# Performance work log

Measured on AMD Instinct MI355X. Metric: run time of the kernel, lower is better.

## Reference

```python
import jax, jax.numpy as jnp
import numpy as np

N = 10000       # nodes
E = 320000      # edges
D = 256         # feature dim (out_channels)
L = 5           # num_layers


def setup_inputs() -> dict:
    key = jax.random.key(0)
    ks = jax.random.split(key, 8)
    x = jax.random.normal(ks[0], (N, D), dtype=jnp.float32)
    edge_index = jax.random.randint(ks[1], (2, E), 0, N, dtype=jnp.int64)
    edge_attr = jax.random.uniform(ks[2], (E,), dtype=jnp.float32)
    s = 1.0 / np.sqrt(D)
    # per-layer message transform weights [L, D, D]
    weight = jax.random.uniform(ks[3], (L, D, D), minval=-s, maxval=s, dtype=jnp.float32)
    # GRUCell parameters (torch layout: [3D, D] rows = r, z, n)
    w_ih = jax.random.uniform(ks[4], (3 * D, D), minval=-s, maxval=s, dtype=jnp.float32)
    w_hh = jax.random.uniform(ks[5], (3 * D, D), minval=-s, maxval=s, dtype=jnp.float32)
    b_ih = jax.random.uniform(ks[6], (3 * D,), minval=-s, maxval=s, dtype=jnp.float32)
    b_hh = jax.random.uniform(ks[7], (3 * D,), minval=-s, maxval=s, dtype=jnp.float32)
    return {"x": x, "edge_index": edge_index, "edge_attr": edge_attr,
            "weight": weight, "w_ih": w_ih, "w_hh": w_hh,
            "b_ih": b_ih, "b_hh": b_hh}


def _gru_cell(inp, h, w_ih, w_hh, b_ih, b_hh):
    # torch.nn.GRUCell math
    gi = inp @ w_ih.T + b_ih    # [N, 3D]
    gh = h @ w_hh.T + b_hh      # [N, 3D]
    i_r, i_z, i_n = jnp.split(gi, 3, axis=-1)
    h_r, h_z, h_n = jnp.split(gh, 3, axis=-1)
    r = jax.nn.sigmoid(i_r + h_r)
    z = jax.nn.sigmoid(i_z + h_z)
    n = jnp.tanh(i_n + r * h_n)
    return (1.0 - z) * n + z * h


def reference(x, edge_index, edge_attr, weight, w_ih, w_hh, b_ih, b_hh):
    src, dst = edge_index[0], edge_index[1]
    h = x
    for l in range(L):
        m = h @ weight[l]                                   # [N, D]
        msg = m[src] * edge_attr[:, None]                   # [E, D]
        agg = jax.ops.segment_sum(msg, dst, num_segments=N)  # [N, D]
        h = _gru_cell(agg, h, w_ih, w_hh, b_ih, b_hh)
    return h
```

## Files before the change

kernel.cpp:

```cpp
#include <hip/hip_runtime.h>
#include <hip/hip_bf16.h>

#define NN 10000
#define NPAD 10048
#define EE 320000
#define DD 256
#define LL 5

typedef __bf16 bf16x8 __attribute__((ext_vector_type(8)));
typedef __bf16 bf16x4 __attribute__((ext_vector_type(4)));
typedef float f32x4 __attribute__((ext_vector_type(4)));

__device__ __forceinline__ void gload_lds16(const void* g, void* l) {
    __builtin_amdgcn_global_load_lds(
        (const __attribute__((address_space(1))) void*)g,
        (__attribute__((address_space(3))) void*)l, 16, 0, 0);
}


__global__ void prep_k(const float* __restrict__ w_hh, const float* __restrict__ x,
                       __bf16* __restrict__ whhb,
                       float* __restrict__ hb, __bf16* __restrict__ hbfA,
                       __bf16* __restrict__ hbfB, __bf16* __restrict__ aggb,
                       int* __restrict__ deg) {
    int i = blockIdx.x * blockDim.x + threadIdx.x;
    if (i < NN * DD) { float v = x[i]; hb[i] = v; hbfA[i] = (__bf16)v; }
    if (i < 768 * 256) whhb[i] = (__bf16)w_hh[i];
    if (i < (NPAD - NN) * DD) {
        hbfA[NN * DD + i] = (__bf16)0.f;
        hbfB[NN * DD + i] = (__bf16)0.f;
        aggb[NN * DD + i] = (__bf16)0.f;
    }
    if (i < NN) deg[i] = 0;
}

__global__ void hist_k(const int* __restrict__ dst, int* __restrict__ deg) {
    int e = blockIdx.x * blockDim.x + threadIdx.x;
    if (e < EE) atomicAdd(&deg[dst[e]], 1);
}

__global__ void scan_k(const int* __restrict__ deg, int* __restrict__ row_start,
                       int* __restrict__ cursor) {
    __shared__ int sums[1024];
    const int CH = 10;
    int t = threadIdx.x;
    int base = t * CH;
    int loc[CH];
    int s = 0;
#pragma unroll
    for (int i = 0; i < CH; i++) {
        int v = (base + i < NN) ? deg[base + i] : 0;
        loc[i] = s;
        s += v;
    }
    sums[t] = s;
    __syncthreads();
    for (int off = 1; off < 1024; off <<= 1) {
        int v = (t >= off) ? sums[t - off] : 0;
        __syncthreads();
        sums[t] += v;
        __syncthreads();
    }
    int pre = (t == 0) ? 0 : sums[t - 1];
#pragma unroll
    for (int i = 0; i < CH; i++) {
        int idx = base + i;
        if (idx < NN) {
            int v = pre + loc[i];
            row_start[idx] = v;
            cursor[idx] = v;
        }
    }
    if (t == 1023) row_start[NN] = sums[1023];
}

__global__ void fill_k(const int* __restrict__ ei, const float* __restrict__ attr,
                       int* __restrict__ cursor, int* __restrict__ ssrc,
                       float* __restrict__ sattr) {
    int e = blockIdx.x * blockDim.x + threadIdx.x;
    if (e < EE) {
        int dv = ei[EE + e];
        int p = atomicAdd(&cursor[dv], 1);
        ssrc[p] = ei[e];
        sattr[p] = attr[e];
    }
}


__global__ __launch_bounds__(256)
void beff32_k(const float* __restrict__ wih, const float* __restrict__ W,
              __bf16* __restrict__ beff) {
    __shared__ float As[16][68];
    __shared__ float Bs[16][68];
    int l = blockIdx.z;
    const float* Wl = W + (size_t)l * DD * DD;
    __bf16* Cl = beff + (size_t)l * 768 * DD;
    int tid = threadIdx.x;
    int tx = tid & 15, ty = tid >> 4;
    int jBase = blockIdx.x * 64;
    int tBase = blockIdx.y * 64;
    int lr = tid >> 2, lq = tid & 3;
    float acc[4][4];
#pragma unroll
    for (int i = 0; i < 4; i++)
#pragma unroll
        for (int j = 0; j < 4; j++) acc[i][j] = 0.f;

    for (int k0 = 0; k0 < DD; k0 += 16) {
        float4 av = *(const float4*)(wih + (size_t)(jBase + lr) * DD + k0 + lq * 4);
        float4 bv = *(const float4*)(Wl + (size_t)(tBase + lr) * DD + k0 + lq * 4);
        __syncthreads();
        As[lq * 4 + 0][lr] = av.x; As[lq * 4 + 1][lr] = av.y;
        As[lq * 4 + 2][lr] = av.z; As[lq * 4 + 3][lr] = av.w;
        Bs[lq * 4 + 0][lr] = bv.x; Bs[lq * 4 + 1][lr] = bv.y;
        Bs[lq * 4 + 2][lr] = bv.z; Bs[lq * 4 + 3][lr] = bv.w;
        __syncthreads();
#pragma unroll
        for (int kk = 0; kk < 16; kk++) {
            float a0 = As[kk][ty * 4 + 0], a1 = As[kk][ty * 4 + 1];
            float a2 = As[kk][ty * 4 + 2], a3 = As[kk][ty * 4 + 3];
            float b0 = Bs[kk][tx * 4 + 0], b1 = Bs[kk][tx * 4 + 1];
            float b2 = Bs[kk][tx * 4 + 2], b3 = Bs[kk][tx * 4 + 3];
            acc[0][0] += a0 * b0; acc[0][1] += a0 * b1; acc[0][2] += a0 * b2; acc[0][3] += a0 * b3;
            acc[1][0] += a1 * b0; acc[1][1] += a1 * b1; acc[1][2] += a1 * b2; acc[1][3] += a1 * b3;
            acc[2][0] += a2 * b0; acc[2][1] += a2 * b1; acc[2][2] += a2 * b2; acc[2][3] += a2 * b3;
            acc[3][0] += a3 * b0; acc[3][1] += a3 * b1; acc[3][2] += a3 * b2; acc[3][3] += a3 * b3;
        }
    }
#pragma unroll
    for (int i = 0; i < 4; i++) {
        int j = jBase + ty * 4 + i;
        bf16x4 o;
        o[0] = (__bf16)acc[i][0]; o[1] = (__bf16)acc[i][1];
        o[2] = (__bf16)acc[i][2]; o[3] = (__bf16)acc[i][3];
        *(bf16x4*)(Cl + (size_t)j * DD + tBase + tx * 4) = o;
    }
}


__global__ __launch_bounds__(256)
void aggregate_bf_k(const __bf16* __restrict__ hsrc, const int* __restrict__ row_start,
                    const int* __restrict__ ssrc, const float* __restrict__ sattr,
                    __bf16* __restrict__ aggb) {
    __shared__ int sIdx[4][64];
    __shared__ float sAtt[4][64];
    int w = threadIdx.x >> 6, lane = threadIdx.x & 63;
    int n = blockIdx.x * 4 + w;
    int s0 = row_start[n], s1 = row_start[n + 1];
    int half = lane >> 5;
    int c8 = (lane & 31) * 8;

    float acc[8] = {0.f, 0.f, 0.f, 0.f, 0.f, 0.f, 0.f, 0.f};

    for (int base = s0; base < s1; base += 64) {
        int cnt = min(64, s1 - base);
        if (lane < cnt) {
            sIdx[w][lane] = ssrc[base + lane];
            sAtt[w][lane] = sattr[base + lane];
        }
        int t = 0;
        for (; t + 8 <= cnt; t += 8) {
#pragma unroll
            for (int u = 0; u < 4; u++) {
                int e = t + u * 2 + half;
                int s = sIdx[w][e];
                float ww = sAtt[w][e];
                bf16x8 v = *(const bf16x8*)(hsrc + (size_t)s * DD + c8);
#pragma unroll
                for (int i = 0; i < 8; i++) acc[i] += (float)v[i] * ww;
            }
        }
        for (; t + 2 <= cnt; t += 2) {
            int e = t + half;
            int s = sIdx[w][e];
            float ww = sAtt[w][e];
            bf16x8 v = *(const bf16x8*)(hsrc + (size_t)s * DD + c8);
#pragma unroll
            for (int i = 0; i < 8; i++) acc[i] += (float)v[i] * ww;
        }
        if (t < cnt && half == 0) {
            int s = sIdx[w][t];
            float ww = sAtt[w][t];
            bf16x8 v = *(const bf16x8*)(hsrc + (size_t)s * DD + c8);
#pragma unroll
            for (int i = 0; i < 8; i++) acc[i] += (float)v[i] * ww;
        }
    }

#pragma unroll
    for (int i = 0; i < 8; i++) acc[i] += __shfl_xor(acc[i], 32, 64);

    if (half == 0) {
        bf16x8 o;
#pragma unroll
        for (int i = 0; i < 8; i++) o[i] = (__bf16)acc[i];
        *(bf16x8*)(aggb + (size_t)n * DD + c8) = o;
    }
}


__global__ __launch_bounds__(512, 2)
void gru_mfma_k(const __bf16* __restrict__ aggb, const __bf16* __restrict__ hbf,
                const float* __restrict__ hin,
                const __bf16* __restrict__ bihw, const __bf16* __restrict__ whh,
                const float* __restrict__ b_ih, const float* __restrict__ b_hh,
                float* __restrict__ hout, __bf16* __restrict__ hbfout) {
    __shared__ __bf16 sA[2][2][64][32];
    __shared__ __bf16 sB[6][2][64][32];
    int tid = threadIdx.x;
    int wave = tid >> 6, lane = tid & 63;
    int ln = lane & 15, quad = lane >> 4;
    int nodeBlock = blockIdx.x * 64;
    int colBlock = blockIdx.y * 64;
    int nf = wave & 3;
    int ch = (wave >> 2) * 32;
    int r4 = lane >> 2;
    int kb = (lane & 3) * 8;

    f32x4 acc[6][2] = {};

    for (int k0 = 0; k0 < DD; k0 += 64) {
        __syncthreads();
#pragma unroll
        for (int ii = 0; ii < 8; ii++) {
            int idx = wave * 8 + ii;
            const __bf16* src;
            __bf16* dst;
            if (idx < 16) {
                int mat = idx >> 3;
                int ksub = (idx >> 2) & 1;
                int rg = idx & 3;
                const __bf16* A = mat ? hbf : aggb;
                src = A + (size_t)(nodeBlock + rg * 16 + r4) * DD + k0 + ksub * 32 + kb;
                dst = &sA[mat][ksub][rg * 16][0];
            } else {
                int j = idx - 16;
                int g6 = j >> 3;
                int ksub = (j >> 2) & 1;
                int rg = j & 3;
                const __bf16* B = (g6 < 3) ? bihw : whh;
                int brow = (g6 % 3) * 256 + colBlock + rg * 16 + r4;
                src = B + (size_t)brow * DD + k0 + ksub * 32 + kb;
                dst = &sB[g6][ksub][rg * 16][0];
            }
            gload_lds16(src, dst);
        }
        __syncthreads();

#pragma unroll
        for (int ksub = 0; ksub < 2; ksub++) {
            bf16x8 aA = *(const bf16x8*)&sA[0][ksub][nf * 16 + ln][quad * 8];
            bf16x8 aH = *(const bf16x8*)&sA[1][ksub][nf * 16 + ln][quad * 8];
#pragma unroll
            for (int g = 0; g < 3; g++) {
#pragma unroll
                for (int cc = 0; cc < 2; cc++) {
                    bf16x8 bI = *(const bf16x8*)&sB[g][ksub][ch + cc * 16 + ln][quad * 8];
                    bf16x8 bH = *(const bf16x8*)&sB[3 + g][ksub][ch + cc * 16 + ln][quad * 8];
                    acc[g][cc] = __builtin_amdgcn_mfma_f32_16x16x32_bf16(aA, bI, acc[g][cc], 0, 0, 0);
                    acc[3 + g][cc] = __builtin_amdgcn_mfma_f32_16x16x32_bf16(aH, bH, acc[3 + g][cc], 0, 0, 0);
                }
            }
        }
    }

#pragma unroll
    for (int r = 0; r < 4; r++) {
        int n = nodeBlock + nf * 16 + quad * 4 + r;
        if (n >= NN) continue;
#pragma unroll
        for (int cc = 0; cc < 2; cc++) {
            int d = colBlock + ch + cc * 16 + ln;
            float ir = acc[0][cc][r] + b_ih[d];
            float iz = acc[1][cc][r] + b_ih[d + 256];
            float in_ = acc[2][cc][r] + b_ih[d + 512];
            float hr = acc[3][cc][r] + b_hh[d];
            float hz = acc[4][cc][r] + b_hh[d + 256];
            float hn = acc[5][cc][r] + b_hh[d + 512];
            float rr = 1.f / (1.f + __expf(-(ir + hr)));
            float zz = 1.f / (1.f + __expf(-(iz + hz)));
            float ax = in_ + rr * hn;
            float e2 = __expf(-2.f * ax);
            float nnv = 2.f / (1.f + e2) - 1.f;
            float hp = hin[(size_t)n * DD + d];
            float o = (1.f - zz) * nnv + zz * hp;
            hout[(size_t)n * DD + d] = o;
            hbfout[(size_t)n * DD + d] = (__bf16)o;
        }
    }
}


extern "C" void kernel_launch(void* const* d_in, const int* in_sizes, int n_in,
                              void* d_out, int out_size, void* d_ws, size_t ws_size,
                              hipStream_t stream) {
    const float* x = (const float*)d_in[0];
    const int* edge_index = (const int*)d_in[1];
    const float* edge_attr = (const float*)d_in[2];
    const float* weight = (const float*)d_in[3];
    const float* w_ih = (const float*)d_in[4];
    const float* w_hh = (const float*)d_in[5];
    const float* b_ih = (const float*)d_in[6];
    const float* b_hh = (const float*)d_in[7];

    size_t off = 0;
    char* base = (char*)d_ws;
    auto carve = [&](size_t bytes) -> void* {
        void* p = base + off;
        off += (bytes + 255) & ~(size_t)255;
        return p;
    };
    float* hb = (float*)carve((size_t)NPAD * DD * 4);
    __bf16* hbfA = (__bf16*)carve((size_t)NPAD * DD * 2);
    __bf16* hbfB = (__bf16*)carve((size_t)NPAD * DD * 2);
    __bf16* aggb = (__bf16*)carve((size_t)NPAD * DD * 2);
    __bf16* whhb = (__bf16*)carve((size_t)768 * DD * 2);
    __bf16* beff = (__bf16*)carve((size_t)LL * 768 * DD * 2);
    int* deg = (int*)carve((size_t)NN * 4);
    int* row_start = (int*)carve((size_t)(NN + 1) * 4);
    int* cursor = (int*)carve((size_t)NN * 4);
    int* ssrc = (int*)carve((size_t)EE * 4);
    float* sattr = (float*)carve((size_t)EE * 4);
    (void)ws_size;

    prep_k<<<(NN * DD + 255) / 256, 256, 0, stream>>>(w_hh, x, whhb, hb, hbfA, hbfB,
                                                      aggb, deg);
    hist_k<<<(EE + 255) / 256, 256, 0, stream>>>(edge_index + EE, deg);
    scan_k<<<1, 1024, 0, stream>>>(deg, row_start, cursor);
    fill_k<<<(EE + 255) / 256, 256, 0, stream>>>(edge_index, edge_attr, cursor, ssrc, sattr);
    beff32_k<<<dim3(12, 4, LL), 256, 0, stream>>>(w_ih, weight, beff);

    float* hA = hb;
    float* hB = (float*)d_out;
    __bf16* hbfIn = hbfA;
    __bf16* hbfOut = hbfB;
    for (int l = 0; l < LL; l++) {
        aggregate_bf_k<<<2500, 256, 0, stream>>>(hbfIn, row_start, ssrc, sattr, aggb);
        gru_mfma_k<<<dim3(157, 4), 512, 0, stream>>>(aggb, hbfIn, hA,
                                                     beff + (size_t)l * 768 * DD, whhb,
                                                     b_ih, b_hh, hB, hbfOut);
        float* t = hA; hA = hB; hB = t;
        __bf16* tb = hbfIn; hbfIn = hbfOut; hbfOut = tb;
    }
}
```

Baseline: 356.7 us.

## Fuse edge aggregation into GRU MFMA kernel, keeping aggregates in LDS

Merges the per-layer aggregation and GRU GEMM kernels into one. Each block gathers neighbour features for 64 nodes into shared memory and preloads the bf16 hidden tile with direct global-to-LDS loads. It then runs the six gate GEMMs with MFMA, reading weight fragments straight from global memory. This removes the bf16 aggregate buffer round trip and one launch per layer. In exchange, the gather is repeated by both column blocks, each wave walks 8 nodes serially, and far fewer waves are available for the latency-bound gather.

```diff
diff --git a/kernel.cpp b/kernel.cpp
--- a/kernel.cpp
+++ b/kernel.cpp
@@ -21,15 +21,13 @@
 __global__ void prep_k(const float* __restrict__ w_hh, const float* __restrict__ x,
                        __bf16* __restrict__ whhb,
                        float* __restrict__ hb, __bf16* __restrict__ hbfA,
-                       __bf16* __restrict__ hbfB, __bf16* __restrict__ aggb,
-                       int* __restrict__ deg) {
+                       __bf16* __restrict__ hbfB, int* __restrict__ deg) {
     int i = blockIdx.x * blockDim.x + threadIdx.x;
     if (i < NN * DD) { float v = x[i]; hb[i] = v; hbfA[i] = (__bf16)v; }
     if (i < 768 * 256) whhb[i] = (__bf16)w_hh[i];
     if (i < (NPAD - NN) * DD) {
         hbfA[NN * DD + i] = (__bf16)0.f;
         hbfB[NN * DD + i] = (__bf16)0.f;
-        aggb[NN * DD + i] = (__bf16)0.f;
     }
     if (i < NN) deg[i] = 0;
 }
@@ -138,128 +136,111 @@
 }
 
 
-__global__ __launch_bounds__(256)
-void aggregate_bf_k(const __bf16* __restrict__ hsrc, const int* __restrict__ row_start,
-                    const int* __restrict__ ssrc, const float* __restrict__ sattr,
-                    __bf16* __restrict__ aggb) {
-    __shared__ int sIdx[4][64];
-    __shared__ float sAtt[4][64];
-    int w = threadIdx.x >> 6, lane = threadIdx.x & 63;
-    int n = blockIdx.x * 4 + w;
-    int s0 = row_start[n], s1 = row_start[n + 1];
-    int half = lane >> 5;
-    int c8 = (lane & 31) * 8;
-
-    float acc[8] = {0.f, 0.f, 0.f, 0.f, 0.f, 0.f, 0.f, 0.f};
-
-    for (int base = s0; base < s1; base += 64) {
-        int cnt = min(64, s1 - base);
-        if (lane < cnt) {
-            sIdx[w][lane] = ssrc[base + lane];
-            sAtt[w][lane] = sattr[base + lane];
-        }
-        int t = 0;
-        for (; t + 8 <= cnt; t += 8) {
-#pragma unroll
-            for (int u = 0; u < 4; u++) {
-                int e = t + u * 2 + half;
-                int s = sIdx[w][e];
-                float ww = sAtt[w][e];
-                bf16x8 v = *(const bf16x8*)(hsrc + (size_t)s * DD + c8);
-#pragma unroll
-                for (int i = 0; i < 8; i++) acc[i] += (float)v[i] * ww;
-            }
-        }
-        for (; t + 2 <= cnt; t += 2) {
-            int e = t + half;
-            int s = sIdx[w][e];
-            float ww = sAtt[w][e];
-            bf16x8 v = *(const bf16x8*)(hsrc + (size_t)s * DD + c8);
-#pragma unroll
-            for (int i = 0; i < 8; i++) acc[i] += (float)v[i] * ww;
-        }
-        if (t < cnt && half == 0) {
-            int s = sIdx[w][t];
-            float ww = sAtt[w][t];
-            bf16x8 v = *(const bf16x8*)(hsrc + (size_t)s * DD + c8);
-#pragma unroll
-            for (int i = 0; i < 8; i++) acc[i] += (float)v[i] * ww;
-        }
-    }
-
-#pragma unroll
-    for (int i = 0; i < 8; i++) acc[i] += __shfl_xor(acc[i], 32, 64);
-
-    if (half == 0) {
-        bf16x8 o;
-#pragma unroll
-        for (int i = 0; i < 8; i++) o[i] = (__bf16)acc[i];
-        *(bf16x8*)(aggb + (size_t)n * DD + c8) = o;
-    }
-}
-
-
-__global__ __launch_bounds__(512, 2)
-void gru_mfma_k(const __bf16* __restrict__ aggb, const __bf16* __restrict__ hbf,
-                const float* __restrict__ hin,
-                const __bf16* __restrict__ bihw, const __bf16* __restrict__ whh,
-                const float* __restrict__ b_ih, const float* __restrict__ b_hh,
-                float* __restrict__ hout, __bf16* __restrict__ hbfout) {
-    __shared__ __bf16 sA[2][2][64][32];
-    __shared__ __bf16 sB[6][2][64][32];
+__global__ __launch_bounds__(512, 4)
+void fused_layer_k(const __bf16* __restrict__ hbf, const float* __restrict__ hin,
+                   const int* __restrict__ row_start, const int* __restrict__ ssrc,
+                   const float* __restrict__ sattr,
+                   const __bf16* __restrict__ bihw, const __bf16* __restrict__ whh,
+                   const float* __restrict__ b_ih, const float* __restrict__ b_hh,
+                   float* __restrict__ hout, __bf16* __restrict__ hbfout) {
+    __shared__ __bf16 aggT[8][64][32];
+    __shared__ __bf16 hT[8][64][32];
+    __shared__ int sIdx[8][64];
+    __shared__ float sAtt[8][64];
+
     int tid = threadIdx.x;
     int wave = tid >> 6, lane = tid & 63;
     int ln = lane & 15, quad = lane >> 4;
     int nodeBlock = blockIdx.x * 64;
-    int colBlock = blockIdx.y * 64;
-    int nf = wave & 3;
-    int ch = (wave >> 2) * 32;
     int r4 = lane >> 2;
     int kb = (lane & 3) * 8;
 
-    f32x4 acc[6][2] = {};
-
-    for (int k0 = 0; k0 < DD; k0 += 64) {
-        __syncthreads();
-#pragma unroll
-        for (int ii = 0; ii < 8; ii++) {
-            int idx = wave * 8 + ii;
-            const __bf16* src;
-            __bf16* dst;
-            if (idx < 16) {
-                int mat = idx >> 3;
-                int ksub = (idx >> 2) & 1;
-                int rg = idx & 3;
-                const __bf16* A = mat ? hbf : aggb;
-                src = A + (size_t)(nodeBlock + rg * 16 + r4) * DD + k0 + ksub * 32 + kb;
-                dst = &sA[mat][ksub][rg * 16][0];
-            } else {
-                int j = idx - 16;
-                int g6 = j >> 3;
-                int ksub = (j >> 2) & 1;
-                int rg = j & 3;
-                const __bf16* B = (g6 < 3) ? bihw : whh;
-                int brow = (g6 % 3) * 256 + colBlock + rg * 16 + r4;
-                src = B + (size_t)brow * DD + k0 + ksub * 32 + kb;
-                dst = &sB[g6][ksub][rg * 16][0];
+#pragma unroll
+    for (int ii = 0; ii < 4; ii++) {
+        int idx = wave * 4 + ii;
+        int rg = idx >> 3;
+        int ksub = idx & 7;
+        const __bf16* src = hbf + (size_t)(nodeBlock + rg * 16 + r4) * DD + ksub * 32 + kb;
+        gload_lds16(src, &hT[ksub][rg * 16][0]);
+    }
+
+    int half = lane >> 5;
+    int c8 = (lane & 31) * 8;
+    int L = lane & 31;
+    for (int nn = 0; nn < 8; nn++) {
+        int nl = wave * 8 + nn;
+        int n = nodeBlock + nl;
+        float acc8[8] = {0.f, 0.f, 0.f, 0.f, 0.f, 0.f, 0.f, 0.f};
+        if (n < NN) {
+            int s0 = row_start[n], s1 = row_start[n + 1];
+            for (int base = s0; base < s1; base += 64) {
+                int cnt = min(64, s1 - base);
+                if (lane < cnt) {
+                    sIdx[wave][lane] = ssrc[base + lane];
+                    sAtt[wave][lane] = sattr[base + lane];
+                }
+                int t = 0;
+                for (; t + 8 <= cnt; t += 8) {
+#pragma unroll
+                    for (int u = 0; u < 4; u++) {
+                        int e = t + u * 2 + half;
+                        int s = sIdx[wave][e];
+                        float ww = sAtt[wave][e];
+                        bf16x8 v = *(const bf16x8*)(hbf + (size_t)s * DD + c8);
+#pragma unroll
+                        for (int i = 0; i < 8; i++) acc8[i] += (float)v[i] * ww;
+                    }
+                }
+                for (; t + 2 <= cnt; t += 2) {
+                    int e = t + half;
+                    int s = sIdx[wave][e];
+                    float ww = sAtt[wave][e];
+                    bf16x8 v = *(const bf16x8*)(hbf + (size_t)s * DD + c8);
+#pragma unroll
+                    for (int i = 0; i < 8; i++) acc8[i] += (float)v[i] * ww;
+                }
+                if (t < cnt && half == 0) {
+                    int s = sIdx[wave][t];
+                    float ww = sAtt[wave][t];
+                    bf16x8 v = *(const bf16x8*)(hbf + (size_t)s * DD + c8);
+#pragma unroll
+                    for (int i = 0; i < 8; i++) acc8[i] += (float)v[i] * ww;
+                }
             }
-            gload_lds16(src, dst);
-        }
-        __syncthreads();
-
-#pragma unroll
-        for (int ksub = 0; ksub < 2; ksub++) {
-            bf16x8 aA = *(const bf16x8*)&sA[0][ksub][nf * 16 + ln][quad * 8];
-            bf16x8 aH = *(const bf16x8*)&sA[1][ksub][nf * 16 + ln][quad * 8];
-#pragma unroll
-            for (int g = 0; g < 3; g++) {
-#pragma unroll
-                for (int cc = 0; cc < 2; cc++) {
-                    bf16x8 bI = *(const bf16x8*)&sB[g][ksub][ch + cc * 16 + ln][quad * 8];
-                    bf16x8 bH = *(const bf16x8*)&sB[3 + g][ksub][ch + cc * 16 + ln][quad * 8];
-                    acc[g][cc] = __builtin_amdgcn_mfma_f32_16x16x32_bf16(aA, bI, acc[g][cc], 0, 0, 0);
-                    acc[3 + g][cc] = __builtin_amdgcn_mfma_f32_16x16x32_bf16(aH, bH, acc[3 + g][cc], 0, 0, 0);
-                }
+#pragma unroll
+            for (int i = 0; i < 8; i++) acc8[i] += __shfl_xor(acc8[i], 32, 64);
+        }
+        if (half == 0) {
+            bf16x8 o;
+#pragma unroll
+            for (int i = 0; i < 8; i++) o[i] = (__bf16)acc8[i];
+            *(bf16x8*)&aggT[L >> 2][nl][(L & 3) * 8] = o;
+        }
+    }
+    __syncthreads();
+
+    int nf = wave & 3;
+    int cg = wave >> 2;
+    int colAbs = blockIdx.y * 128 + cg * 64;
+
+    f32x4 acc[6][4] = {};
+
+    const __bf16* pI = bihw + (size_t)(colAbs + ln) * DD + quad * 8;
+    const __bf16* pH = whh + (size_t)(colAbs + ln) * DD + quad * 8;
+
+    for (int ksub = 0; ksub < 8; ksub++) {
+        bf16x8 aA = *(const bf16x8*)&aggT[ksub][nf * 16 + ln][quad * 8];
+        bf16x8 aH = *(const bf16x8*)&hT[ksub][nf * 16 + ln][quad * 8];
+        int ko = ksub * 32;
+#pragma unroll
+        for (int g = 0; g < 3; g++) {
+#pragma unroll
+            for (int cc = 0; cc < 4; cc++) {
+                size_t roff = (size_t)(g * 256 + cc * 16) * DD + ko;
+                bf16x8 bI = *(const bf16x8*)(pI + roff);
+                bf16x8 bH = *(const bf16x8*)(pH + roff);
+                acc[g][cc] = __builtin_amdgcn_mfma_f32_16x16x32_bf16(aA, bI, acc[g][cc], 0, 0, 0);
+                acc[3 + g][cc] = __builtin_amdgcn_mfma_f32_16x16x32_bf16(aH, bH, acc[3 + g][cc], 0, 0, 0);
             }
         }
     }
@@ -269,8 +250,8 @@
         int n = nodeBlock + nf * 16 + quad * 4 + r;
         if (n >= NN) continue;
 #pragma unroll
-        for (int cc = 0; cc < 2; cc++) {
-            int d = colBlock + ch + cc * 16 + ln;
+        for (int cc = 0; cc < 4; cc++) {
+            int d = colAbs + cc * 16 + ln;
             float ir = acc[0][cc][r] + b_ih[d];
             float iz = acc[1][cc][r] + b_ih[d + 256];
             float in_ = acc[2][cc][r] + b_ih[d + 512];
@@ -313,7 +294,6 @@
     float* hb = (float*)carve((size_t)NPAD * DD * 4);
     __bf16* hbfA = (__bf16*)carve((size_t)NPAD * DD * 2);
     __bf16* hbfB = (__bf16*)carve((size_t)NPAD * DD * 2);
-    __bf16* aggb = (__bf16*)carve((size_t)NPAD * DD * 2);
     __bf16* whhb = (__bf16*)carve((size_t)768 * DD * 2);
     __bf16* beff = (__bf16*)carve((size_t)LL * 768 * DD * 2);
     int* deg = (int*)carve((size_t)NN * 4);
@@ -323,8 +303,7 @@
     float* sattr = (float*)carve((size_t)EE * 4);
     (void)ws_size;
 
-    prep_k<<<(NN * DD + 255) / 256, 256, 0, stream>>>(w_hh, x, whhb, hb, hbfA, hbfB,
-                                                      aggb, deg);
+    prep_k<<<(NN * DD + 255) / 256, 256, 0, stream>>>(w_hh, x, whhb, hb, hbfA, hbfB, deg);
     hist_k<<<(EE + 255) / 256, 256, 0, stream>>>(edge_index + EE, deg);
     scan_k<<<1, 1024, 0, stream>>>(deg, row_start, cursor);
     fill_k<<<(EE + 255) / 256, 256, 0, stream>>>(edge_index, edge_attr, cursor, ssrc, sattr);
@@ -335,10 +314,9 @@
     __bf16* hbfIn = hbfA;
     __bf16* hbfOut = hbfB;
     for (int l = 0; l < LL; l++) {
-        aggregate_bf_k<<<2500, 256, 0, stream>>>(hbfIn, row_start, ssrc, sattr, aggb);
-        gru_mfma_k<<<dim3(157, 4), 512, 0, stream>>>(aggb, hbfIn, hA,
-                                                     beff + (size_t)l * 768 * DD, whhb,
-                                                     b_ih, b_hh, hB, hbfOut);
+        fused_layer_k<<<dim3(157, 2), 512, 0, stream>>>(hbfIn, hA, row_start, ssrc, sattr,
+                                                        beff + (size_t)l * 768 * DD, whhb,
+                                                        b_ih, b_hh, hB, hbfOut);
         float* t = hA; hA = hB; hB = t;
         __bf16* tb = hbfIn; hbfIn = hbfOut; hbfOut = tb;
     }
```

Result: slower. 1.053 ms (+195.1%).
